# Kernel optimization log

Hardware: AMD Instinct MI355X
Metric: run time of the kernel (lower is better)

Reference implementation:

```python
import jax, jax.numpy as jnp
import numpy as np

N, E, D_IN, H, DH = 50000, 800000, 128, 4, 32
NEG_SLOPE = 0.01  # torch nn.LeakyReLU() default
EPS = 1e-16       # torch_geometric softmax epsilon


def setup_inputs() -> dict:
    key = jax.random.key(0)
    k0, k1, k2, k3, k4 = jax.random.split(key, 5)
    x = jax.random.normal(k0, (N, D_IN), dtype=jnp.float32)
    edge_index = jax.random.randint(k1, (2, E), 0, N, dtype=jnp.int64)
    # Glorot-uniform-ish scales
    s_proj = (6.0 / (D_IN + H * DH)) ** 0.5
    W_proj = jax.random.uniform(k2, (D_IN, H * DH), jnp.float32, -s_proj, s_proj)
    s_att = (6.0 / (H + 2 * DH)) ** 0.5
    att_w = jax.random.uniform(k3, (H, 2 * DH), jnp.float32, -s_att, s_att)
    W_skip = jax.random.uniform(k4, (D_IN, H * DH), jnp.float32, -s_proj, s_proj)
    return {"x": x, "W_proj": W_proj, "att_w": att_w, "W_skip": W_skip,
            "edge_index": edge_index}


def reference(x, W_proj, att_w, W_skip, edge_index):
    num_nodes = x.shape[0]
    h = (x @ W_proj).reshape(num_nodes, H, DH)          # [N,H,Dh]
    src, dst = edge_index[0], edge_index[1]
    h_src = h[src]                                      # [E,H,Dh] gather
    h_dst = h[dst]                                      # [E,H,Dh] gather
    # einsum('nah,nah->na', cat([h_src,h_dst],-1), a) == split-a form:
    a_src, a_dst = att_w[:, :DH], att_w[:, DH:]
    e = (jnp.einsum('ehd,hd->eh', h_src, a_src)
         + jnp.einsum('ehd,hd->eh', h_dst, a_dst))      # [E,H]
    e = jax.nn.leaky_relu(e, NEG_SLOPE)
    # segment softmax grouped by dst (max-stabilized, as in torch_geometric)
    e_max = jax.ops.segment_max(e, dst, num_segments=num_nodes)  # [N,H]
    e_exp = jnp.exp(e - e_max[dst])
    denom = jax.ops.segment_sum(e_exp, dst, num_segments=num_nodes)
    alpha = e_exp / (denom[dst] + EPS)                  # [E,H]
    # scatter-add aggregation (index_add_ by dst)
    h_prime = jax.ops.segment_sum(alpha[..., None] * h_src, dst,
                                  num_segments=num_nodes)  # [N,H,Dh]
    h_prime = h_prime + (x @ W_skip).reshape(num_nodes, H, DH)
    return h_prime.reshape(num_nodes, H * DH)
```

## Files before the change

kernel.cpp:

```cpp
#include <hip/hip_runtime.h>
#include <hip/hip_bf16.h>

#define N_NODES 50000
#define E_EDGES 800000
#define NHEAD 4
#define DHEAD 32
#define DOUT 128
#define NEG_SLOPE 0.01f
#define EPS_F 1e-16f
#define DMAX 256
#define ELP 264
#define NB 196
#define CAP 8192

typedef __attribute__((ext_vector_type(8))) short bf16x8;
typedef __attribute__((ext_vector_type(4))) float f32x4;

__device__ __forceinline__ float bf2f(unsigned short u) {
    return __uint_as_float((unsigned)u << 16);
}
__device__ __forceinline__ unsigned short f2bf(float f) {
    return __bfloat16_as_ushort(__float2bfloat16(f));
}

__device__ __forceinline__ void load_edge(const int* __restrict__ ei, int isI64,
                                          int e, int& src, int& dst) {
    if (isI64) { src = ei[2 * e]; dst = ei[2 * (E_EDGES + e)]; }
    else       { src = ei[e];     dst = ei[E_EDGES + e]; }
}

__global__ __launch_bounds__(128) void k_prep(const float* __restrict__ Wp,
                                              const float* __restrict__ Ws,
                                              const int* __restrict__ ei,
                                              unsigned short* __restrict__ Wt,
                                              int* __restrict__ flag) {
    int b = blockIdx.x;
    if (b < 256) {
        int c = b, k = threadIdx.x;
        float v = (c < DOUT) ? Wp[k * DOUT + c] : Ws[k * DOUT + (c - DOUT)];
        int nf = c >> 4, cl = c & 15;
        int ks = k >> 5, r = k & 31, lq = r >> 3, e = r & 7;
        Wt[(((nf * 4 + ks) << 6) + lq * 16 + cl) * 8 + e] = f2bf(v);
    } else {
        __shared__ int cnt;
        if (threadIdx.x == 0) cnt = 0;
        __syncthreads();
        int nz = 0;
        #pragma unroll
        for (int k2 = 0; k2 < 16; ++k2) {
            int pos = (threadIdx.x + k2 * 128) * 2 + 1;
            if (ei[pos] != 0) nz = 1;
        }
        if (nz) atomicOr(&cnt, 1);
        __syncthreads();
        if (threadIdx.x == 0) *flag = (cnt == 0) ? 1 : 0;
    }
}

#define HBP 136
#define SKP 132
__global__ __launch_bounds__(256) void k_gemm(const float* __restrict__ x,
                                              const unsigned short* __restrict__ Wt,
                                              const float* __restrict__ att,
                                              unsigned short* __restrict__ hb,
                                              float* __restrict__ as_,
                                              float* __restrict__ ad_,
                                              float* __restrict__ out) {
    __shared__ float SK[64 * SKP];
    __shared__ unsigned short HB[64 * HBP];
    char* XSc = (char*)SK;

    const int tid = threadIdx.x;
    const int rw  = tid >> 6;
    const int l   = tid & 63;
    const int l15 = l & 15;
    const int lq  = l >> 4;

    {
        int d = tid * 16;
        #pragma unroll
        for (int it = 0; it < 8; ++it, d += 4096) {
            int row = d >> 9, col = d & 511;
            int grow = blockIdx.x * 64 + row;
            if (grow > N_NODES - 1) grow = N_NODES - 1;
            float4 v = *(const float4*)((const char*)x + (size_t)grow * 512 + col);
            *(float4*)(XSc + (row << 9) + (col ^ ((row & 7) << 4))) = v;
        }
    }
    __syncthreads();

    const int rl = rw * 16 + l15;
    const int sw = (rl & 7) << 4;
    bf16x8 afr[4];
    #pragma unroll
    for (int ks = 0; ks < 4; ++ks) {
        int c0 = ks * 128 + lq * 32;
        float4 u0 = *(const float4*)(XSc + (rl << 9) + (c0 ^ sw));
        float4 u1 = *(const float4*)(XSc + (rl << 9) + ((c0 + 16) ^ sw));
        bf16x8 a;
        a[0] = (short)f2bf(u0.x); a[1] = (short)f2bf(u0.y);
        a[2] = (short)f2bf(u0.z); a[3] = (short)f2bf(u0.w);
        a[4] = (short)f2bf(u1.x); a[5] = (short)f2bf(u1.y);
        a[6] = (short)f2bf(u1.z); a[7] = (short)f2bf(u1.w);
        afr[ks] = a;
    }
    __syncthreads();

    f32x4 acc[16];
    #pragma unroll
    for (int nf = 0; nf < 16; ++nf) acc[nf] = (f32x4)(0.0f);

    #pragma unroll
    for (int nf = 0; nf < 16; ++nf) {
        #pragma unroll
        for (int ks = 0; ks < 4; ++ks) {
            bf16x8 b = *(const bf16x8*)(Wt + ((((nf * 4 + ks) << 6) + l) << 3));
            acc[nf] = __builtin_amdgcn_mfma_f32_16x16x32_bf16(afr[ks], b, acc[nf], 0, 0, 0);
        }
    }

    #pragma unroll
    for (int nf = 0; nf < 8; ++nf) {
        #pragma unroll
        for (int q = 0; q < 4; ++q) {
            int r2 = rw * 16 + lq * 4 + q;
            HB[r2 * HBP + nf * 16 + l15] = f2bf(acc[nf][q]);
        }
    }
    #pragma unroll
    for (int nf = 8; nf < 16; ++nf) {
        #pragma unroll
        for (int q = 0; q < 4; ++q) {
            int r2 = rw * 16 + lq * 4 + q;
            SK[r2 * SKP + (nf - 8) * 16 + l15] = acc[nf][q];
        }
    }
    __syncthreads();

    {
        int rl2 = tid >> 2, hd = tid & 3;
        const unsigned* HBu = (const unsigned*)HB;
        const float* a1 = att + hd * 2 * DHEAD;
        const float* a2 = a1 + DHEAD;
        float s1 = 0.0f, s2 = 0.0f;
        #pragma unroll
        for (int j = 0; j < 16; ++j) {
            unsigned u = HBu[rl2 * (HBP / 2) + hd * 16 + j];
            float lo = bf2f((unsigned short)(u & 0xffff));
            float hi = bf2f((unsigned short)(u >> 16));
            s1 += lo * a1[2 * j] + hi * a1[2 * j + 1];
            s2 += lo * a2[2 * j] + hi * a2[2 * j + 1];
        }
        int rowg = blockIdx.x * 64 + rl2;
        as_[(size_t)rowg * 4 + hd] = s1;
        ad_[(size_t)rowg * 4 + hd] = s2;
    }

    {
        const unsigned* HBu = (const unsigned*)HB;
        #pragma unroll
        for (int it = 0; it < 4; ++it) {
            int idx = it * 256 + tid;
            int row = idx >> 4, g = idx & 15;
            int wb = row * (HBP / 2) + g * 4;
            uint4 v;
            v.x = HBu[wb]; v.y = HBu[wb + 1]; v.z = HBu[wb + 2]; v.w = HBu[wb + 3];
            *(uint4*)(hb + ((size_t)(blockIdx.x * 64 + row)) * DOUT + g * 8) = v;
        }
    }
    {
        #pragma unroll
        for (int it = 0; it < 8; ++it) {
            int idx = it * 256 + tid;
            int row = idx >> 5, c4 = idx & 31;
            int rowg = blockIdx.x * 64 + row;
            if (rowg < N_NODES) {
                float4 v = *(const float4*)&SK[row * SKP + c4 * 4];
                *(float4*)(out + (size_t)rowg * DOUT + c4 * 4) = v;
            }
        }
    }
}

__global__ __launch_bounds__(256) void k_part(const int* __restrict__ ei,
                                              const int* __restrict__ flag,
                                              int* __restrict__ bucketCnt,
                                              unsigned* __restrict__ payload) {
    __shared__ int hist[NB];
    __shared__ int curs[NB];
    const int t = threadIdx.x;
    const int base = blockIdx.x * 3125;
    const int isI64 = *flag;

    for (int i = t; i < NB; i += 256) hist[i] = 0;
    __syncthreads();
    for (int i = t; i < 3125; i += 256) {
        int src, dst;
        load_edge(ei, isI64, base + i, src, dst);
        if ((unsigned)dst < N_NODES) atomicAdd(&hist[dst >> 8], 1);
    }
    __syncthreads();
    for (int i = t; i < NB; i += 256)
        curs[i] = atomicAdd(&bucketCnt[i], hist[i]);
    __syncthreads();
    for (int i = t; i < 3125; i += 256) {
        int src, dst;
        load_edge(ei, isI64, base + i, src, dst);
        if ((unsigned)src >= N_NODES || (unsigned)dst >= N_NODES) continue;
        int b = dst >> 8;
        int pos = atomicAdd(&curs[b], 1);
        if (pos < CAP)
            payload[((size_t)b << 13) + pos] = ((unsigned)(dst & 255) << 16) | (unsigned)src;
    }
}

__global__ __launch_bounds__(256) void k_csr(const int* __restrict__ bucketCnt,
                                             const unsigned* __restrict__ payload,
                                             int* __restrict__ deg,
                                             int* __restrict__ ofs,
                                             int* __restrict__ srcs) {
    __shared__ int h[256];
    __shared__ int cur[256];
    __shared__ int sc[256];
    const int b = blockIdx.x;
    const int t = threadIdx.x;
    int cnt = bucketCnt[b];
    if (cnt > CAP) cnt = CAP;
    const unsigned* __restrict__ pl = payload + ((size_t)b << 13);

    h[t] = 0;
    __syncthreads();
    for (int i = t; i < cnt; i += 256) atomicAdd(&h[pl[i] >> 16], 1);
    __syncthreads();
    int v = h[t];
    sc[t] = v;
    __syncthreads();
    #pragma unroll
    for (int off = 1; off < 256; off <<= 1) {
        int u = (t >= off) ? sc[t - off] : 0;
        __syncthreads();
        sc[t] += u;
        __syncthreads();
    }
    int ex = sc[t] - v;
    cur[t] = ex;
    int n = (b << 8) + t;
    if (n < N_NODES) { deg[n] = v; ofs[n] = (b << 13) + ex; }
    __syncthreads();
    for (int i = t; i < cnt; i += 256) {
        unsigned p = pl[i];
        int pos = atomicAdd(&cur[p >> 16], 1);
        srcs[((size_t)b << 13) + pos] = (int)(p & 0xFFFFu);
    }
}

__global__ __launch_bounds__(128) void k_gat(const int* __restrict__ ofs,
                                             const int* __restrict__ deg,
                                             const int* __restrict__ srcs,
                                             const float* __restrict__ as_,
                                             const float* __restrict__ ad_,
                                             const unsigned short* __restrict__ hb,
                                             float* __restrict__ out) {
    __shared__ float EL[2][NHEAD * ELP];
    __shared__ int   SRC[2][DMAX];

    const int sub = threadIdx.x >> 6;
    const int k   = threadIdx.x & 63;
    const int hd  = k >> 4;
    const int l16 = k & 15;
    const int n = blockIdx.x * 2 + sub;
    const int o = ofs[n];
    const int d = deg[n];
    const unsigned* __restrict__ hbu = (const unsigned*)hb;
    float* ELn = EL[sub];
    int*   SRCn = SRC[sub];

    int fast = __syncthreads_and(d <= DMAX);

    if (fast) {
        const float4 adv4 = *(const float4*)(ad_ + (size_t)n * 4);
        for (int e = k; e < d; e += 64) {
            int s = srcs[o + e];
            SRCn[e] = s;
            float4 a4 = *(const float4*)(as_ + (size_t)s * 4);
            float e0 = a4.x + adv4.x, e1 = a4.y + adv4.y;
            float e2 = a4.z + adv4.z, e3 = a4.w + adv4.w;
            ELn[0 * ELP + e] = (e0 > 0.0f) ? e0 : NEG_SLOPE * e0;
            ELn[1 * ELP + e] = (e1 > 0.0f) ? e1 : NEG_SLOPE * e1;
            ELn[2 * ELP + e] = (e2 > 0.0f) ? e2 : NEG_SLOPE * e2;
            ELn[3 * ELP + e] = (e3 > 0.0f) ? e3 : NEG_SLOPE * e3;
        }
        __syncthreads();
        float m = -3.4e38f;
        for (int i = l16; i < d; i += 16) m = fmaxf(m, ELn[hd * ELP + i]);
        #pragma unroll
        for (int off = 8; off; off >>= 1) m = fmaxf(m, __shfl_xor(m, off));
        float den = 0.0f;
        for (int i = l16; i < d; i += 16) {
            float p = __expf(ELn[hd * ELP + i] - m);
            ELn[hd * ELP + i] = p;
            den += p;
        }
        #pragma unroll
        for (int off = 8; off; off >>= 1) den += __shfl_xor(den, off);
        __syncthreads();
        float num0 = 0.0f, num1 = 0.0f;
        for (int i = 0; i < d; ++i) {
            float p = ELn[hd * ELP + i];
            int s = SRCn[i];
            unsigned u = hbu[(size_t)s * (DOUT / 2) + k];
            num0 = fmaf(p, bf2f((unsigned short)(u & 0xffff)), num0);
            num1 = fmaf(p, bf2f((unsigned short)(u >> 16)), num1);
        }
        float inv = 1.0f / (den + EPS_F);
        float2* op = (float2*)(out + (size_t)n * DOUT + 2 * k);
        float2 sk = *op;
        *op = make_float2(num0 * inv + sk.x, num1 * inv + sk.y);
    } else {
        const float adv = ad_[(size_t)n * 4 + hd];
        float m = -3.4e38f;
        for (int i = 0; i < d; ++i) {
            float el = as_[(size_t)srcs[o + i] * 4 + hd] + adv;
            el = (el > 0.0f) ? el : NEG_SLOPE * el;
            m = fmaxf(m, el);
        }
        float den = 0.0f, num0 = 0.0f, num1 = 0.0f;
        for (int i = 0; i < d; ++i) {
            int s = srcs[o + i];
            float el = as_[(size_t)s * 4 + hd] + adv;
            el = (el > 0.0f) ? el : NEG_SLOPE * el;
            float p = __expf(el - m);
            den += p;
            unsigned u = hbu[(size_t)s * (DOUT / 2) + k];
            num0 = fmaf(p, bf2f((unsigned short)(u & 0xffff)), num0);
            num1 = fmaf(p, bf2f((unsigned short)(u >> 16)), num1);
        }
        float inv = 1.0f / (den + EPS_F);
        float2* op = (float2*)(out + (size_t)n * DOUT + 2 * k);
        float2 sk = *op;
        *op = make_float2(num0 * inv + sk.x, num1 * inv + sk.y);
    }
}

extern "C" void kernel_launch(void* const* d_in, const int* in_sizes, int n_in,
                              void* d_out, int out_size, void* d_ws, size_t ws_size,
                              hipStream_t stream) {
    const float* x   = (const float*)d_in[0];
    const float* Wp  = (const float*)d_in[1];
    const float* att = (const float*)d_in[2];
    const float* Ws  = (const float*)d_in[3];
    const int*   ei  = (const int*)d_in[4];
    float* out = (float*)d_out;

    char* ws = (char*)d_ws;
    unsigned short* hb        = (unsigned short*)(ws);
    unsigned short* Wt        = (unsigned short*)(ws + 12812288);
    float*          as_       = (float*)(ws + 12877824);
    float*          ad_       = (float*)(ws + 13678592);
    int*            deg       = (int*)(ws + 14479360);
    int*            ofs       = (int*)(ws + 14680064);
    unsigned*       payload   = (unsigned*)(ws + 14880768);
    int*            srcs      = (int*)(ws + 21303296);
    int*            bucketCnt = (int*)(ws + 27725824);
    int*            flag      = (int*)(ws + 27726848);

    hipMemsetAsync(bucketCnt, 0, NB * 4, stream);

    k_prep<<<257, 128, 0, stream>>>(Wp, Ws, ei, Wt, flag);
    k_gemm<<<(N_NODES + 63) / 64, 256, 0, stream>>>(x, Wt, att, hb, as_, ad_, out);
    k_part<<<256, 256, 0, stream>>>(ei, flag, bucketCnt, payload);
    k_csr<<<NB, 256, 0, stream>>>(bucketCnt, payload, deg, ofs, srcs);
    k_gat<<<N_NODES / 2, 128, 0, stream>>>(ofs, deg, srcs, as_, ad_, hb, out);
}
```

Baseline: 118.4 us.

## Pack src offset with softmax weight and split edges across half-waves

```diff
diff --git a/kernel.cpp b/kernel.cpp
--- a/kernel.cpp
+++ b/kernel.cpp
@@ -9,7 +9,7 @@
 #define NEG_SLOPE 0.01f
 #define EPS_F 1e-16f
 #define DMAX 256
-#define ELP 264
+#define POP 265
 #define NB 196
 #define CAP 8192
 
@@ -261,19 +261,21 @@
                                              const float* __restrict__ ad_,
                                              const unsigned short* __restrict__ hb,
                                              float* __restrict__ out) {
-    __shared__ float EL[2][NHEAD * ELP];
-    __shared__ int   SRC[2][DMAX];
+    __shared__ uint2 PO[2][NHEAD * POP];
+    __shared__ float DEN[2][NHEAD];
 
     const int sub = threadIdx.x >> 6;
     const int k   = threadIdx.x & 63;
     const int hd  = k >> 4;
     const int l16 = k & 15;
+    const int half = k >> 5;
+    const int c8   = k & 31;
+    const int hd4  = c8 >> 3;
     const int n = blockIdx.x * 2 + sub;
     const int o = ofs[n];
     const int d = deg[n];
-    const unsigned* __restrict__ hbu = (const unsigned*)hb;
-    float* ELn = EL[sub];
-    int*   SRCn = SRC[sub];
+    uint2* POn = PO[sub];
+    float* POf = (float*)POn;
 
     int fast = __syncthreads_and(d <= DMAX);
 
@@ -281,42 +283,61 @@
         const float4 adv4 = *(const float4*)(ad_ + (size_t)n * 4);
         for (int e = k; e < d; e += 64) {
             int s = srcs[o + e];
-            SRCn[e] = s;
+            unsigned off = (unsigned)s << 8;
             float4 a4 = *(const float4*)(as_ + (size_t)s * 4);
             float e0 = a4.x + adv4.x, e1 = a4.y + adv4.y;
             float e2 = a4.z + adv4.z, e3 = a4.w + adv4.w;
-            ELn[0 * ELP + e] = (e0 > 0.0f) ? e0 : NEG_SLOPE * e0;
-            ELn[1 * ELP + e] = (e1 > 0.0f) ? e1 : NEG_SLOPE * e1;
-            ELn[2 * ELP + e] = (e2 > 0.0f) ? e2 : NEG_SLOPE * e2;
-            ELn[3 * ELP + e] = (e3 > 0.0f) ? e3 : NEG_SLOPE * e3;
+            e0 = (e0 > 0.0f) ? e0 : NEG_SLOPE * e0;
+            e1 = (e1 > 0.0f) ? e1 : NEG_SLOPE * e1;
+            e2 = (e2 > 0.0f) ? e2 : NEG_SLOPE * e2;
+            e3 = (e3 > 0.0f) ? e3 : NEG_SLOPE * e3;
+            POn[0 * POP + e] = make_uint2(off, __float_as_uint(e0));
+            POn[1 * POP + e] = make_uint2(off, __float_as_uint(e1));
+            POn[2 * POP + e] = make_uint2(off, __float_as_uint(e2));
+            POn[3 * POP + e] = make_uint2(off, __float_as_uint(e3));
         }
         __syncthreads();
         float m = -3.4e38f;
-        for (int i = l16; i < d; i += 16) m = fmaxf(m, ELn[hd * ELP + i]);
+        for (int i = l16; i < d; i += 16) m = fmaxf(m, POf[(hd * POP + i) * 2 + 1]);
         #pragma unroll
         for (int off = 8; off; off >>= 1) m = fmaxf(m, __shfl_xor(m, off));
         float den = 0.0f;
         for (int i = l16; i < d; i += 16) {
-            float p = __expf(ELn[hd * ELP + i] - m);
-            ELn[hd * ELP + i] = p;
+            float p = __expf(POf[(hd * POP + i) * 2 + 1] - m);
+            POf[(hd * POP + i) * 2 + 1] = p;
             den += p;
         }
         #pragma unroll
         for (int off = 8; off; off >>= 1) den += __shfl_xor(den, off);
-        __syncthreads();
-        float num0 = 0.0f, num1 = 0.0f;
-        for (int i = 0; i < d; ++i) {
-            float p = ELn[hd * ELP + i];
-            int s = SRCn[i];
-            unsigned u = hbu[(size_t)s * (DOUT / 2) + k];
-            num0 = fmaf(p, bf2f((unsigned short)(u & 0xffff)), num0);
-            num1 = fmaf(p, bf2f((unsigned short)(u >> 16)), num1);
-        }
-        float inv = 1.0f / (den + EPS_F);
-        float2* op = (float2*)(out + (size_t)n * DOUT + 2 * k);
-        float2 sk = *op;
-        *op = make_float2(num0 * inv + sk.x, num1 * inv + sk.y);
+        if (l16 == 0) DEN[sub][hd] = den;
+        __syncthreads();
+        float4 num = make_float4(0.0f, 0.0f, 0.0f, 0.0f);
+        const uint2* POh = POn + hd4 * POP;
+        for (int it = 0; 2 * it < d; ++it) {
+            int i = 2 * it + half;
+            if (i < d) {
+                uint2 po = POh[i];
+                float p = __uint_as_float(po.y);
+                uint2 u = *(const uint2*)((const char*)hb + po.x + c8 * 8);
+                num.x = fmaf(p, bf2f((unsigned short)(u.x & 0xffff)), num.x);
+                num.y = fmaf(p, bf2f((unsigned short)(u.x >> 16)), num.y);
+                num.z = fmaf(p, bf2f((unsigned short)(u.y & 0xffff)), num.z);
+                num.w = fmaf(p, bf2f((unsigned short)(u.y >> 16)), num.w);
+            }
+        }
+        num.x += __shfl_xor(num.x, 32);
+        num.y += __shfl_xor(num.y, 32);
+        num.z += __shfl_xor(num.z, 32);
+        num.w += __shfl_xor(num.w, 32);
+        if (half == 0) {
+            float inv = 1.0f / (DEN[sub][hd4] + EPS_F);
+            float4* op = (float4*)(out + (size_t)n * DOUT + c8 * 4);
+            float4 sk = *op;
+            *op = make_float4(num.x * inv + sk.x, num.y * inv + sk.y,
+                              num.z * inv + sk.z, num.w * inv + sk.w);
+        }
     } else {
+        const unsigned* __restrict__ hbu = (const unsigned*)hb;
         const float adv = ad_[(size_t)n * 4 + hd];
         float m = -3.4e38f;
         for (int i = 0; i < d; ++i) {
```

New measurement: 147.9 us. 1.25x slower.
